# Kernel tuning notes

Hardware: AMD Instinct MI355X
Metric: run time of the kernel (lower is better)

## Reference

```python
import jax, jax.numpy as jnp
import numpy as np

VOCAB = 32000
HIDDEN = 256
GO_IDX = VOCAB - 1  # 'GO' appended last to i2w


def setup_inputs() -> dict:
    key = jax.random.key(0)
    ks = jax.random.split(key, 10)
    L, B, H, V = 64, 128, HIDDEN, VOCAB
    s = 1.0 / np.sqrt(H)
    return {
        "outputs": jax.random.randint(ks[0], (L, B), 0, V, dtype=jnp.int64),
        "h0": jax.random.normal(ks[1], (B, H), dtype=jnp.float32),
        "c0": jax.random.normal(ks[2], (B, H), dtype=jnp.float32),
        "batch_size": B,
        "embed_W": jax.random.normal(ks[3], (V, H), dtype=jnp.float32),
        "W_ih": jax.random.uniform(ks[4], (4 * H, H), jnp.float32, -s, s),
        "W_hh": jax.random.uniform(ks[5], (4 * H, H), jnp.float32, -s, s),
        "b_ih": jax.random.uniform(ks[6], (4 * H,), jnp.float32, -s, s),
        "b_hh": jax.random.uniform(ks[7], (4 * H,), jnp.float32, -s, s),
        "proj_W": jax.random.uniform(ks[8], (V, H), jnp.float32, -s, s),
        "proj_b": jax.random.uniform(ks[9], (V,), jnp.float32, -s, s),
    }


def _lstm_cell(x, h, c, W_ih, W_hh, b_ih, b_hh):
    # PyTorch LSTMCell: gates ordered (i, f, g, o)
    gates = x @ W_ih.T + h @ W_hh.T + (b_ih + b_hh)  # [B, 4H]
    i, f, g, o = jnp.split(gates, 4, axis=-1)
    c_new = jax.nn.sigmoid(f) * c + jax.nn.sigmoid(i) * jnp.tanh(g)
    h_new = jax.nn.sigmoid(o) * jnp.tanh(c_new)
    return h_new, c_new


def reference(outputs, h0, c0, batch_size, embed_W, W_ih, W_hh, b_ih, b_hh, proj_W, proj_b):
    L = outputs.shape[0]
    dec_emb = embed_W[outputs]  # [L, B, H]
    GO_emb = jnp.broadcast_to(embed_W[GO_IDX], (batch_size, HIDDEN))
    # step 0: GO token
    h, c = _lstm_cell(GO_emb, h0, c0, W_ih, W_hh, b_ih, b_hh)
    # steps 1..L-1: teacher forcing with dec_emb[i+1] (random.random() > 0 is always True)
    def step(carry, x):
        h, c = carry
        h, c = _lstm_cell(x, h, c, W_ih, W_hh, b_ih, b_hh)
        return (h, c), h
    (_, _), hs = jax.lax.scan(step, (h, c), dec_emb[1:])  # [L-1, B, H]
    pred = jnp.concatenate([h[None], hs], axis=0)  # [L, B, H]
    logits = pred.reshape(L * batch_size, HIDDEN) @ proj_W.T + proj_b
    return logits.reshape(L, batch_size, VOCAB)
```

## Files before the change

### kernel.cpp

```cpp
#include <hip/hip_runtime.h>
#include <stdint.h>

#define LSTEPS 64
#define BATCH 128
#define HID 256
#define NGATES 1024
#define NVOCAB 32000
#define GO_TOK 31999

typedef __bf16 bf16x8 __attribute__((ext_vector_type(8)));
typedef float f32x4 __attribute__((ext_vector_type(4)));
typedef unsigned short u16;
typedef u16 u16x8 __attribute__((ext_vector_type(8)));

#define GLDS16(gp, lp)                                                          \
  __builtin_amdgcn_global_load_lds(                                             \
      (const __attribute__((address_space(1))) void*)(gp),                      \
      (__attribute__((address_space(3))) void*)(lp), 16, 0, 0)

__device__ __forceinline__ u16 f2bf(float f) {
  union { float f; uint32_t u; } v; v.f = f;
  uint32_t u = v.u;
  return (u16)((u + 0x7FFFu + ((u >> 16) & 1u)) >> 16);
}
__device__ __forceinline__ float sigm(float x) {
  return 1.0f / (1.0f + __expf(-x));
}
__device__ __forceinline__ float tanh_f(float x) {
  return 2.0f / (1.0f + __expf(-2.0f * x)) - 1.0f;
}

__global__ void k_pack(const float* __restrict__ src, u16* __restrict__ dst, int J) {
  int j = blockIdx.x * 256 + threadIdx.x;
  int kb = blockIdx.y;
  const float* s = src + (size_t)j * HID + kb * 8;
  u16x8 o;
#pragma unroll
  for (int e = 0; e < 8; ++e) o[e] = f2bf(s[e]);
  *reinterpret_cast<u16x8*>(dst + ((size_t)kb * J + j) * 8) = o;
}

__global__ void k_pack2(const float* __restrict__ src, u16* __restrict__ dst) {
  int i = blockIdx.x * 256 + threadIdx.x;
  const float* s = src + (size_t)i * 8;
  u16x8 o;
#pragma unroll
  for (int e = 0; e < 8; ++e) o[e] = f2bf(s[e]);
  *reinterpret_cast<u16x8*>(dst + (size_t)i * 8) = o;
}

__global__ void k_bsum(const float* __restrict__ a, const float* __restrict__ b, float* __restrict__ o) {
  int i = blockIdx.x * 256 + threadIdx.x;
  o[i] = a[i] + b[i];
}

__global__ void k_gather(const int* __restrict__ outs, const float* __restrict__ embW, u16* __restrict__ X) {
  int idx = blockIdx.x * 256 + threadIdx.x;
  int r = idx >> 5, k8 = idx & 31;
  int t = r >> 7;
  int src = (t == 0) ? GO_TOK : outs[r];
  const float* p = embW + (size_t)src * HID + k8 * 8;
  u16x8 o;
#pragma unroll
  for (int e = 0; e < 8; ++e) o[e] = f2bf(p[e]);
  *reinterpret_cast<u16x8*>(X + (size_t)r * HID + k8 * 8) = o;
}

__global__ __launch_bounds__(256, 2) void k_gemm(const u16* __restrict__ A, const u16* __restrict__ Bp,
                                                 const float* __restrict__ bias, float* __restrict__ C,
                                                 int N) {
  __shared__ __align__(16) u16 sA[64 * 256];
  __shared__ __align__(16) u16 sB[32 * 64 * 8];
  const int tid = threadIdx.x;
  const int m0 = blockIdx.y * 64;
  const int n0 = blockIdx.x * 64;
#pragma unroll
  for (int i = 0; i < 8; ++i) {
    int idx = tid + i * 256;
    int r = idx >> 5, k8 = idx & 31;
    *reinterpret_cast<uint4*>(&sA[(r * 32 + (k8 ^ (r & 7))) * 8]) =
        *reinterpret_cast<const uint4*>(&A[(size_t)(m0 + r) * HID + k8 * 8]);
  }
#pragma unroll
  for (int i = 0; i < 8; ++i) {
    int idx = tid + i * 256;
    int kb = idx >> 6, j = idx & 63;
    *reinterpret_cast<uint4*>(&sB[(kb * 64 + (j ^ ((kb & 3) << 2))) * 8]) =
        *reinterpret_cast<const uint4*>(&Bp[((size_t)kb * N + n0 + j) * 8]);
  }
  __syncthreads();
  const int wave = tid >> 6, lane = tid & 63;
  const int wm = wave >> 1, wn = wave & 1;
  const int lr = lane & 15, lk = lane >> 4;
  f32x4 acc[2][2] = {};
#pragma unroll
  for (int kk = 0; kk < 8; ++kk) {
    bf16x8 a[2], b[2];
    int k8 = kk * 4 + lk;
#pragma unroll
    for (int mt = 0; mt < 2; ++mt) {
      int r = wm * 32 + mt * 16 + lr;
      a[mt] = *reinterpret_cast<const bf16x8*>(&sA[(r * 32 + (k8 ^ (r & 7))) * 8]);
    }
#pragma unroll
    for (int nt = 0; nt < 2; ++nt) {
      int j = wn * 32 + nt * 16 + lr;
      b[nt] = *reinterpret_cast<const bf16x8*>(&sB[(k8 * 64 + (j ^ ((k8 & 3) << 2))) * 8]);
    }
#pragma unroll
    for (int mt = 0; mt < 2; ++mt)
#pragma unroll
      for (int nt = 0; nt < 2; ++nt)
        acc[mt][nt] = __builtin_amdgcn_mfma_f32_16x16x32_bf16(a[mt], b[nt], acc[mt][nt], 0, 0, 0);
  }
#pragma unroll
  for (int mt = 0; mt < 2; ++mt) {
#pragma unroll
    for (int nt = 0; nt < 2; ++nt) {
      int col = n0 + wn * 32 + nt * 16 + lr;
      float bs = bias[col];
#pragma unroll
      for (int i = 0; i < 4; ++i) {
        int row = m0 + wm * 32 + mt * 16 + lk * 4 + i;
        C[(size_t)row * N + col] = acc[mt][nt][i] + bs;
      }
    }
  }
}

__global__ __launch_bounds__(512) void k_fused(const float* __restrict__ G,
                                               const u16* __restrict__ WhhTp,
                                               const float* __restrict__ h0,
                                               const float* __restrict__ c0,
                                               u16* __restrict__ h_all,
                                               u16* __restrict__ hx,
                                               unsigned* __restrict__ flags,
                                               unsigned* __restrict__ donecnt,
                                               const u16* __restrict__ projW,
                                               const float* __restrict__ projb,
                                               float* __restrict__ out) {
  __shared__ __align__(16) char smem[163840];
  const int tid = threadIdx.x;
  const int w = tid >> 6, lane = tid & 63;
  const int lr = lane & 15, lk = lane >> 4;

  if (blockIdx.x < 16) {
    u16* sh = (u16*)smem;
    float(*sg)[516] = (float(*)[516])(smem + 8192);
    const int bid = blockIdx.x;
    const int bg = bid & 7, hh = bid >> 3, ph = hh ^ 1;

    bf16x8 whhA[4][4], whhB[4][4];
    int jg_[4];
#pragma unroll
    for (int nt = 0; nt < 4; ++nt) {
      int j = w * 64 + nt * 16 + lr;
      int jg = (j >> 7) * 256 + hh * 128 + (j & 127);
      jg_[nt] = jg;
#pragma unroll
      for (int kk = 0; kk < 4; ++kk) {
        int k8A = hh * 16 + kk * 4 + lk;
        int k8B = ph * 16 + kk * 4 + lk;
        whhA[nt][kk] = *reinterpret_cast<const bf16x8*>(&WhhTp[((size_t)k8A * NGATES + jg) * 8]);
        whhB[nt][kk] = *reinterpret_cast<const bf16x8*>(&WhhTp[((size_t)k8B * NGATES + jg) * 8]);
      }
    }
    const int b = tid >> 5, d4 = (tid & 31) * 4;
    f32x4 cc = *reinterpret_cast<const f32x4*>(&c0[(size_t)(bg * 16 + b) * HID + hh * 128 + d4]);
    {
      int r = tid >> 5, c8 = tid & 31;
      const float* p = h0 + (size_t)(bg * 16 + r) * HID + c8 * 8;
      u16x8 o;
#pragma unroll
      for (int e = 0; e < 8; ++e) o[e] = f2bf(p[e]);
      *reinterpret_cast<u16x8*>(&sh[(r * 32 + (c8 ^ (r & 7))) * 8]) = o;
    }
    __syncthreads();

    for (int t = 0; t < LSTEPS; ++t) {
      float gv[4][4];
#pragma unroll
      for (int nt = 0; nt < 4; ++nt)
#pragma unroll
        for (int i = 0; i < 4; ++i)
          gv[nt][i] = G[((size_t)t * BATCH + bg * 16 + lk * 4 + i) * NGATES + jg_[nt]];

      f32x4 acc[4] = {};
      {
        bf16x8 ah[4];
#pragma unroll
        for (int kk = 0; kk < 4; ++kk) {
          int c8 = hh * 16 + kk * 4 + lk;
          ah[kk] = *reinterpret_cast<const bf16x8*>(&sh[(lr * 32 + (c8 ^ (lr & 7))) * 8]);
        }
#pragma unroll
        for (int kk = 0; kk < 4; ++kk)
#pragma unroll
          for (int nt = 0; nt < 4; ++nt)
            acc[nt] = __builtin_amdgcn_mfma_f32_16x16x32_bf16(ah[kk], whhA[nt][kk], acc[nt], 0, 0, 0);
      }
      if (t == 0) {
        bf16x8 ah[4];
#pragma unroll
        for (int kk = 0; kk < 4; ++kk) {
          int c8 = ph * 16 + kk * 4 + lk;
          ah[kk] = *reinterpret_cast<const bf16x8*>(&sh[(lr * 32 + (c8 ^ (lr & 7))) * 8]);
        }
#pragma unroll
        for (int kk = 0; kk < 4; ++kk)
#pragma unroll
          for (int nt = 0; nt < 4; ++nt)
            acc[nt] = __builtin_amdgcn_mfma_f32_16x16x32_bf16(ah[kk], whhB[nt][kk], acc[nt], 0, 0, 0);
      } else {
        {
          const unsigned* f = &flags[(bid ^ 8) * 16];
          int it = 0;
          unsigned v;
          do {
            v = __hip_atomic_load(f, __ATOMIC_ACQUIRE, __HIP_MEMORY_SCOPE_AGENT);
          } while (v < (unsigned)t && ++it < (1 << 22));
        }
        bf16x8 ah[4];
#pragma unroll
        for (int kk = 0; kk < 4; ++kk)
          ah[kk] = *reinterpret_cast<const bf16x8*>(
              hx + (((t - 1) & 1) * BATCH + bg * 16 + lr) * HID + ph * 128 + (kk * 4 + lk) * 8);
#pragma unroll
        for (int kk = 0; kk < 4; ++kk)
#pragma unroll
          for (int nt = 0; nt < 4; ++nt)
            acc[nt] = __builtin_amdgcn_mfma_f32_16x16x32_bf16(ah[kk], whhB[nt][kk], acc[nt], 0, 0, 0);
      }
#pragma unroll
      for (int nt = 0; nt < 4; ++nt) {
        int j = w * 64 + nt * 16 + lr;
#pragma unroll
        for (int i = 0; i < 4; ++i) sg[lk * 4 + i][j] = acc[nt][i] + gv[nt][i];
      }
      __syncthreads();
      {
        f32x4 ig = *reinterpret_cast<const f32x4*>(&sg[b][d4]);
        f32x4 fg = *reinterpret_cast<const f32x4*>(&sg[b][128 + d4]);
        f32x4 gg = *reinterpret_cast<const f32x4*>(&sg[b][256 + d4]);
        f32x4 og = *reinterpret_cast<const f32x4*>(&sg[b][384 + d4]);
        u16 hb[4];
#pragma unroll
        for (int e = 0; e < 4; ++e) {
          float cn = sigm(fg[e]) * cc[e] + sigm(ig[e]) * tanh_f(gg[e]);
          cc[e] = cn;
          hb[e] = f2bf(sigm(og[e]) * tanh_f(cn));
        }
        uint2 hp;
        hp.x = (unsigned)hb[0] | ((unsigned)hb[1] << 16);
        hp.y = (unsigned)hb[2] | ((unsigned)hb[3] << 16);
        int c8 = hh * 16 + (d4 >> 3);
        *reinterpret_cast<uint2*>(&sh[(b * 32 + (c8 ^ (b & 7))) * 8 + (d4 & 7)]) = hp;
        *reinterpret_cast<uint2*>(&hx[((t & 1) * BATCH + bg * 16 + b) * HID + hh * 128 + d4]) = hp;
        unsigned long long hv = ((unsigned long long)hp.y << 32) | (unsigned long long)hp.x;
        __hip_atomic_store(
            (unsigned long long*)(h_all + ((size_t)t * BATCH + bg * 16 + b) * HID + hh * 128 + d4),
            hv, __ATOMIC_RELAXED, __HIP_MEMORY_SCOPE_AGENT);
      }
      __syncthreads();
      if (tid == 0) {
        __hip_atomic_store(&flags[bid * 16], (unsigned)(t + 1), __ATOMIC_RELEASE,
                           __HIP_MEMORY_SCOPE_AGENT);
        __hip_atomic_fetch_add(&donecnt[t * 16], 1u, __ATOMIC_RELEASE, __HIP_MEMORY_SCOPE_AGENT);
      }
    }
  } else {
    u16* sB = (u16*)smem;
    u16* sA = (u16*)(smem + 131072);
    const int p = blockIdx.x - 16;
    const int n0 = p * 256;
    const int wm = w >> 2, wn = w & 3;

#pragma unroll
    for (int i = 0; i < 16; ++i) {
      int c = i * 512 + tid;
      int row = c >> 5, cl = c & 31, scc = cl ^ (row & 7);
      GLDS16(&projW[(size_t)(n0 + row) * HID + scc * 8], &sB[c * 8]);
    }
    float bs[4];
#pragma unroll
    for (int nt = 0; nt < 4; ++nt) bs[nt] = projb[n0 + wn * 64 + nt * 16 + lr];
    __syncthreads();

    for (int t = 0; t < LSTEPS; ++t) {
      const size_t m0 = (size_t)t * 128;
      if (tid == 0) {
        int it = 0;
        unsigned v;
        do {
          v = __hip_atomic_load(&donecnt[t * 16], __ATOMIC_RELAXED, __HIP_MEMORY_SCOPE_AGENT);
          if (v >= 16u) break;
          __builtin_amdgcn_s_sleep(8);
        } while (++it < (1 << 20));
        (void)__hip_atomic_load(&donecnt[t * 16], __ATOMIC_ACQUIRE, __HIP_MEMORY_SCOPE_AGENT);
      }
      __syncthreads();

#define ASTAGE(bsel, ks)                                                        \
      {                                                                         \
        _Pragma("unroll") for (int i = 0; i < 2; ++i) {                         \
          int c = i * 512 + tid;                                                \
          int row = c >> 3, cl = c & 7, scc = cl ^ (row & 7);                   \
          GLDS16(&h_all[(m0 + row) * HID + (ks) * 64 + scc * 8],                \
                 &sA[(bsel) * 8192 + c * 8]);                                   \
        }                                                                       \
      }

      ASTAGE(0, 0)
      __syncthreads();
      f32x4 acc[4][4] = {};
      int buf = 0;
#pragma unroll
      for (int ks = 0; ks < 4; ++ks) {
        if (ks < 3) ASTAGE(buf ^ 1, ks + 1)
        const u16* sAc = &sA[buf * 8192];
#pragma unroll
        for (int kk = 0; kk < 2; ++kk) {
          bf16x8 a[4], bb[4];
#pragma unroll
          for (int mt = 0; mt < 4; ++mt) {
            int r = wm * 64 + mt * 16 + lr;
            a[mt] = *reinterpret_cast<const bf16x8*>(&sAc[(r * 8 + ((kk * 4 + lk) ^ (r & 7))) * 8]);
          }
#pragma unroll
          for (int nt = 0; nt < 4; ++nt) {
            int r = wn * 64 + nt * 16 + lr;
            int k8g = ks * 8 + kk * 4 + lk;
            bb[nt] = *reinterpret_cast<const bf16x8*>(&sB[(r * 32 + (k8g ^ (r & 7))) * 8]);
          }
#pragma unroll
          for (int mt = 0; mt < 4; ++mt)
#pragma unroll
            for (int nt = 0; nt < 4; ++nt)
              acc[mt][nt] =
                  __builtin_amdgcn_mfma_f32_16x16x32_bf16(a[mt], bb[nt], acc[mt][nt], 0, 0, 0);
        }
        __syncthreads();
        buf ^= 1;
      }
#undef ASTAGE

#pragma unroll
      for (int mt = 0; mt < 4; ++mt) {
#pragma unroll
        for (int i = 0; i < 4; ++i) {
          size_t row = m0 + wm * 64 + mt * 16 + lk * 4 + i;
          float* cp = &out[row * NVOCAB + n0 + wn * 64];
#pragma unroll
          for (int nt = 0; nt < 4; ++nt)
            __builtin_nontemporal_store(acc[mt][nt][i] + bs[nt], &cp[nt * 16 + lr]);
        }
      }
    }
  }
}

extern "C" void kernel_launch(void* const* d_in, const int* in_sizes, int n_in,
                              void* d_out, int out_size, void* d_ws, size_t ws_size,
                              hipStream_t stream) {
  const int* outs = (const int*)d_in[0];
  const float* h0 = (const float*)d_in[1];
  const float* c0 = (const float*)d_in[2];
  const float* embW = (const float*)d_in[4];
  const float* W_ih = (const float*)d_in[5];
  const float* W_hh = (const float*)d_in[6];
  const float* b_ih = (const float*)d_in[7];
  const float* b_hh = (const float*)d_in[8];
  const float* proj_W = (const float*)d_in[9];
  const float* proj_b = (const float*)d_in[10];
  float* out = (float*)d_out;

  char* ws = (char*)d_ws;
  u16* Xbf      = (u16*)(ws + 0);
  u16* WihTp    = (u16*)(ws + 4194304);
  u16* WhhTp    = (u16*)(ws + 4718592);
  u16* projWbf  = (u16*)(ws + 5242880);
  u16* h_all    = (u16*)(ws + 21626880);
  u16* hx       = (u16*)(ws + 25821184);
  float* bsum   = (float*)(ws + 25952256);
  unsigned* flags   = (unsigned*)(ws + 25956352);
  unsigned* donecnt = (unsigned*)(ws + 25957376);
  float* G      = (float*)(ws + 25961472);

  hipMemsetAsync(flags, 0, 5120, stream);
  k_pack<<<dim3(4, 32), 256, 0, stream>>>(W_ih, WihTp, NGATES);
  k_pack<<<dim3(4, 32), 256, 0, stream>>>(W_hh, WhhTp, NGATES);
  k_pack2<<<dim3(4000), 256, 0, stream>>>(proj_W, projWbf);
  k_bsum<<<dim3(4), 256, 0, stream>>>(b_ih, b_hh, bsum);
  k_gather<<<dim3(1024), 256, 0, stream>>>(outs, embW, Xbf);
  k_gemm<<<dim3(16, 128), 256, 0, stream>>>(Xbf, WihTp, bsum, G, NGATES);
  k_fused<<<dim3(141), 512, 0, stream>>>(G, WhhTp, h0, c0, h_all, hx, flags, donecnt,
                                         projWbf, proj_b, out);
}
```

Baseline: 439.0 us.

## Read projection A operand directly from global and replace barriers with LDS flag

In the projection blocks, the double-buffered LDS staging of h_all tiles and the per-k-step __syncthreads are removed. A fragments are now loaded straight from global memory (L2-resident h_all). The per-timestep barrier after the global done-count poll becomes an LDS flag that thread 0 sets and other waves spin on, so waves are not held together by workgroup barriers. This cuts barrier and staging overhead, at the cost of redundant global loads across waves and uncoalesced 16-byte row reads.

```diff
diff --git a/kernel.cpp b/kernel.cpp
--- a/kernel.cpp
+++ b/kernel.cpp
@@ -270,7 +270,7 @@
     }
   } else {
     u16* sB = (u16*)smem;
-    u16* sA = (u16*)(smem + 131072);
+    unsigned* tflag = (unsigned*)(smem + 131072);
     const int p = blockIdx.x - 16;
     const int n0 = p * 256;
     const int wm = w >> 2, wn = w & 3;
@@ -284,10 +284,11 @@
     float bs[4];
 #pragma unroll
     for (int nt = 0; nt < 4; ++nt) bs[nt] = projb[n0 + wn * 64 + nt * 16 + lr];
+    if (tid == 0)
+      __hip_atomic_store(tflag, 0u, __ATOMIC_RELAXED, __HIP_MEMORY_SCOPE_WORKGROUP);
     __syncthreads();
 
     for (int t = 0; t < LSTEPS; ++t) {
-      const size_t m0 = (size_t)t * 128;
       if (tid == 0) {
         int it = 0;
         unsigned v;
@@ -297,39 +298,33 @@
           __builtin_amdgcn_s_sleep(8);
         } while (++it < (1 << 20));
         (void)__hip_atomic_load(&donecnt[t * 16], __ATOMIC_ACQUIRE, __HIP_MEMORY_SCOPE_AGENT);
-      }
-      __syncthreads();
-
-#define ASTAGE(bsel, ks)                                                        \
-      {                                                                         \
-        _Pragma("unroll") for (int i = 0; i < 2; ++i) {                         \
-          int c = i * 512 + tid;                                                \
-          int row = c >> 3, cl = c & 7, scc = cl ^ (row & 7);                   \
-          GLDS16(&h_all[(m0 + row) * HID + (ks) * 64 + scc * 8],                \
-                 &sA[(bsel) * 8192 + c * 8]);                                   \
-        }                                                                       \
-      }
-
-      ASTAGE(0, 0)
-      __syncthreads();
+        __hip_atomic_store(tflag, (unsigned)(t + 1), __ATOMIC_RELEASE,
+                           __HIP_MEMORY_SCOPE_WORKGROUP);
+      }
+      {
+        int it = 0;
+        while (__hip_atomic_load(tflag, __ATOMIC_ACQUIRE, __HIP_MEMORY_SCOPE_WORKGROUP) <
+                   (unsigned)(t + 1) &&
+               ++it < (1 << 22))
+          __builtin_amdgcn_s_sleep(2);
+      }
+
+      const size_t m0 = (size_t)t * 128;
       f32x4 acc[4][4] = {};
-      int buf = 0;
 #pragma unroll
       for (int ks = 0; ks < 4; ++ks) {
-        if (ks < 3) ASTAGE(buf ^ 1, ks + 1)
-        const u16* sAc = &sA[buf * 8192];
 #pragma unroll
         for (int kk = 0; kk < 2; ++kk) {
+          int k8g = ks * 8 + kk * 4 + lk;
           bf16x8 a[4], bb[4];
 #pragma unroll
           for (int mt = 0; mt < 4; ++mt) {
             int r = wm * 64 + mt * 16 + lr;
-            a[mt] = *reinterpret_cast<const bf16x8*>(&sAc[(r * 8 + ((kk * 4 + lk) ^ (r & 7))) * 8]);
+            a[mt] = *reinterpret_cast<const bf16x8*>(&h_all[(m0 + r) * HID + (size_t)k8g * 8]);
           }
 #pragma unroll
           for (int nt = 0; nt < 4; ++nt) {
             int r = wn * 64 + nt * 16 + lr;
-            int k8g = ks * 8 + kk * 4 + lk;
             bb[nt] = *reinterpret_cast<const bf16x8*>(&sB[(r * 32 + (k8g ^ (r & 7))) * 8]);
           }
 #pragma unroll
@@ -339,10 +334,7 @@
               acc[mt][nt] =
                   __builtin_amdgcn_mfma_f32_16x16x32_bf16(a[mt], bb[nt], acc[mt][nt], 0, 0, 0);
         }
-        __syncthreads();
-        buf ^= 1;
-      }
-#undef ASTAGE
+      }
 
 #pragma unroll
       for (int mt = 0; mt < 4; ++mt) {
@@ -386,7 +378,7 @@
   unsigned* donecnt = (unsigned*)(ws + 25957376);
   float* G      = (float*)(ws + 25961472);
 
-  hipMemsetAsync(flags, 0, 5120, stream);
+  (void)hipMemsetAsync(flags, 0, 5120, stream);
   k_pack<<<dim3(4, 32), 256, 0, stream>>>(W_ih, WihTp, NGATES);
   k_pack<<<dim3(4, 32), 256, 0, stream>>>(W_hh, WhhTp, NGATES);
   k_pack2<<<dim3(4000), 256, 0, stream>>>(proj_W, projWbf);
```

New measurement: 626.7 us. 1.43x slower.
